# Optimization experiments

Measured on AMD Instinct MI355X. Metric: run time of the kernel, lower is better.

## Reference

```python
import jax, jax.numpy as jnp
import numpy as np

B, D1, D2, D3 = 4, 64, 64, 64
CIN, COUT = 32, 32
M1, M2, M3 = 8, 8, 8


def setup_inputs() -> dict:
    key = jax.random.key(0)
    k1, k2, k3 = jax.random.split(key, 3)
    x = jax.random.normal(k1, (B, D1, D2, D3, CIN), dtype=jnp.float32)
    # scale ~ random_normal initializer (stddev 0.05 default in keras)
    w_real = jax.random.normal(k2, (CIN, COUT, M1, M2, M3), dtype=jnp.float32) * 0.05
    w_imag = jax.random.normal(k3, (CIN, COUT, M1, M2, M3), dtype=jnp.float32) * 0.05
    return {"x": x, "w_real": w_real, "w_imag": w_imag}


def reference(x, w_real, w_imag):
    # tf.signal.fft3d transforms the innermost 3 dims of [B,D1,D2,D3,C]
    x_ft = jnp.fft.fftn(x.astype(jnp.complex64), axes=(2, 3, 4))
    # low-mode truncation over axes 1,2,3 (as in the original code)
    x_low = x_ft[:, :M1, :M2, :M3, :]                       # [B,M1,M2,M3,CIN]
    w = (w_real + 1j * w_imag).astype(jnp.complex64)         # [CIN,COUT,M1,M2,M3]
    x_low = jnp.transpose(x_low, (0, 4, 1, 2, 3))            # [B,CIN,M1,M2,M3]
    # Faithful to original: i,j of weights are summed out, k is matched.
    out_low = jnp.einsum('bcmnk,coijk->bomnk', x_low, w)     # [B,COUT,M1,M2,M3]
    out_low = jnp.transpose(out_low, (0, 2, 3, 4, 1))        # [B,M1,M2,M3,COUT]
    # zero-padded spectrum (replaces the wasteful tensor_scatter_nd_update)
    out_ft = jnp.zeros((B, D1, D2, D3, COUT), dtype=jnp.complex64)
    out_ft = out_ft.at[:, :M1, :M2, :M3, :].set(out_low)
    y = jnp.fft.ifftn(out_ft, axes=(2, 3, 4))
    return jnp.real(y).astype(jnp.float32)
```

## Files before the change

### kernel.cpp

```cpp
#include <hip/hip_runtime.h>


#define PI2F 6.28318530717958647692f

typedef float vf4 __attribute__((ext_vector_type(4)));

__device__ __forceinline__ float2 cmul(float2 a, float2 b) {
    return make_float2(a.x * b.x - a.y * b.y, a.x * b.y + a.y * b.x);
}

__global__ void k_weff(const float* __restrict__ wr, const float* __restrict__ wi,
                       float2* __restrict__ Weff) {
    __shared__ float2 ls[256];
    int t = threadIdx.x;
    int eL = t & 31, ijg = t >> 5;
    int e = blockIdx.x * 32 + eL;
    int base = (e >> 3) * 512 + (e & 7) + ijg * 64;
    float sr = 0.f, si = 0.f;
    #pragma unroll
    for (int j = 0; j < 8; ++j) { sr += wr[base + j * 8]; si += wi[base + j * 8]; }
    ls[t] = make_float2(sr, si);
    __syncthreads();
    if (t < 32) {
        float2 a = ls[t];
        #pragma unroll
        for (int g = 1; g < 8; ++g) { float2 v = ls[g * 32 + t]; a.x += v.x; a.y += v.y; }
        Weff[blockIdx.x * 32 + t] = a;
    }
}

__global__ void k_T(const float2* __restrict__ Weff, float2* __restrict__ T) {
    __shared__ float2 tw32[32];
    __shared__ float2 P[1024];
    __shared__ float2 A[256];
    int t = threadIdx.x;
    int c = blockIdx.x;
    if (t < 32) {
        float s, co_;
        __sincosf((PI2F / 32.f) * (float)t, &s, &co_);
        tw32[t] = make_float2(co_, s);
    }
    __syncthreads();
    {
        int g = t >> 8, rem = t & 255;
        float2 acc = make_float2(0.f, 0.f);
        #pragma unroll
        for (int k = 0; k < 8; ++k) {
            int fc = g * 8 + k;
            float2 v = Weff[fc * 256 + rem];
            float2 e = tw32[(fc * c) & 31];
            acc.x += v.x * e.x + v.y * e.y;
            acc.y += v.y * e.x - v.x * e.y;
        }
        P[t] = acc;
    }
    __syncthreads();
    if (t < 256) {
        float2 a = P[t];
        #pragma unroll
        for (int g = 1; g < 4; ++g) { float2 v = P[g * 256 + t]; a.x += v.x; a.y += v.y; }
        A[t] = a;
    }
    __syncthreads();
    {
        int g = t >> 8, rem = t & 255;
        int f3 = rem >> 5, co = rem & 31;
        float2 acc = make_float2(0.f, 0.f);
        #pragma unroll
        for (int k = 0; k < 8; ++k) {
            int o = g * 8 + k;
            float2 v = A[o * 8 + f3];
            float2 e = tw32[(o * co) & 31];
            acc.x += v.x * e.x - v.y * e.y;
            acc.y += v.x * e.y + v.y * e.x;
        }
        P[t] = acc;
    }
    __syncthreads();
    if (t < 256) {
        float2 a = P[t];
        #pragma unroll
        for (int g = 1; g < 4; ++g) { float2 v = P[g * 256 + t]; a.x += v.x; a.y += v.y; }
        T[c * 256 + t] = a;
    }
}

__global__ void k_dft2(const float* __restrict__ x, float2* __restrict__ S1) {
    __shared__ float2 tw64[64];
    __shared__ float2 P[2048];
    int t = threadIdx.x;
    int gid = blockIdx.x;
    int d3 = gid & 63, s = gid >> 6;
    int b = s >> 3, d1 = s & 7;
    int c = t & 31, d2g = t >> 5;
    if (t < 64) {
        float sn, cs;
        __sincosf((PI2F / 64.f) * (float)t, &sn, &cs);
        tw64[t] = make_float2(cs, sn);
    }
    __syncthreads();
    const float* xp = x + (size_t)b * 8388608 + (size_t)d1 * 131072 + d3 * 32 + c;
    float2 acc[8];
    #pragma unroll
    for (int f2 = 0; f2 < 8; ++f2) acc[f2] = make_float2(0.f, 0.f);
    #pragma unroll
    for (int k = 0; k < 8; ++k) {
        int d2 = d2g * 8 + k;
        float v = xp[d2 * 2048];
        #pragma unroll
        for (int f2 = 0; f2 < 8; ++f2) {
            float2 e = tw64[(f2 * d2) & 63];
            acc[f2].x += v * e.x;
            acc[f2].y -= v * e.y;
        }
    }
    #pragma unroll
    for (int f2 = 0; f2 < 8; ++f2) P[(d2g * 8 + f2) * 32 + c] = acc[f2];
    __syncthreads();
    {
        int f2 = t >> 5, cc = t & 31;
        float2 a = make_float2(0.f, 0.f);
        #pragma unroll
        for (int g = 0; g < 8; ++g) {
            float2 v = P[(g * 8 + f2) * 32 + cc];
            a.x += v.x; a.y += v.y;
        }
        S1[(size_t)(s * 8 + f2) * 2048 + d3 * 32 + cc] = a;
    }
}

__global__ void k_mid3(const float2* __restrict__ S1, const float2* __restrict__ T,
                       float2* __restrict__ S6) {
    __shared__ float2 sl1[2048];
    __shared__ float2 P[1024];
    __shared__ float2 s2[256];
    __shared__ float2 s5[256];
    __shared__ float2 tw[64];
    int t = threadIdx.x;
    int gid = blockIdx.x;
    if (t < 64) {
        float sn, cs;
        __sincosf((PI2F / 64.f) * (float)t, &sn, &cs);
        tw[t] = make_float2(cs, sn);
    }
    {
        const float4* src = (const float4*)(S1 + (size_t)gid * 2048);
        ((float4*)sl1)[t] = src[t];
    }
    __syncthreads();
    {
        int g = t >> 8, rem = t & 255;
        int f3 = rem >> 5, c = rem & 31;
        float2 a = make_float2(0.f, 0.f);
        #pragma unroll 4
        for (int k = 0; k < 16; ++k) {
            int d3 = g * 16 + k;
            float2 v = sl1[d3 * 32 + c];
            float2 e = tw[(f3 * d3) & 63];
            a.x += v.x * e.x + v.y * e.y;
            a.y += v.y * e.x - v.x * e.y;
        }
        P[t] = a;
    }
    __syncthreads();
    if (t < 256) {
        float2 a = P[t];
        #pragma unroll
        for (int g = 1; g < 4; ++g) { float2 v = P[g * 256 + t]; a.x += v.x; a.y += v.y; }
        s2[t] = a;
    }
    __syncthreads();
    {
        int g = t >> 8, rem = t & 255;
        int f3 = rem >> 5, co = rem & 31;
        float2 a = make_float2(0.f, 0.f);
        #pragma unroll
        for (int k = 0; k < 8; ++k) {
            int cc = g * 8 + k;
            float2 v = s2[f3 * 32 + cc];
            float2 w = T[cc * 256 + f3 * 32 + co];
            a.x += v.x * w.x - v.y * w.y;
            a.y += v.x * w.y + v.y * w.x;
        }
        P[t] = a;
    }
    __syncthreads();
    if (t < 256) {
        float2 a = P[t];
        #pragma unroll
        for (int g = 1; g < 4; ++g) { float2 v = P[g * 256 + t]; a.x += v.x; a.y += v.y; }
        s5[t] = a;
    }
    __syncthreads();
    {
        int co = t & 31, d3a = t >> 5;
        float2* outp = S6 + (size_t)gid * 2048;
        #pragma unroll
        for (int h = 0; h < 2; ++h) {
            int d3 = d3a + 32 * h;
            float2 a = make_float2(0.f, 0.f);
            #pragma unroll
            for (int f3 = 0; f3 < 8; ++f3) {
                float2 v = s5[f3 * 32 + co];
                float2 e = tw[(f3 * d3) & 63];
                a.x += v.x * e.x - v.y * e.y;
                a.y += v.x * e.y + v.y * e.x;
            }
            outp[d3 * 32 + co] = a;
        }
    }
}

__global__ void k_final2(const float2* __restrict__ S6, float* __restrict__ out) {
    __shared__ float2 ls[2048];
    __shared__ float2 tw[64];
    int t = threadIdx.x;
    int gid = blockIdx.x;
    int blk = gid & 7;
    int d1  = (gid >> 3) & 63;
    int b   = gid >> 9;
    int co4 = t & 7;
    int d3r = (t >> 3) & 7;
    int d2q = t >> 6;
    float* obase = out + (size_t)b * 8388608 + (size_t)d1 * 131072
                 + (blk * 8 + d3r) * 32 + co4 * 4;
    if (d1 >= 8) {
        vf4 z = {0.f, 0.f, 0.f, 0.f};
        #pragma unroll
        for (int i = 0; i < 16; ++i) {
            int d2 = d2q * 16 + i;
            __builtin_nontemporal_store(z, (vf4*)(obase + d2 * 2048));
        }
        return;
    }
    if (t < 64) {
        float sn, cs;
        __sincosf((PI2F / 64.f) * (float)t, &sn, &cs);
        tw[t] = make_float2(cs, sn);
    }
    {
        const float4* src = (const float4*)(S6 + (size_t)(b * 8 + d1) * 16384);
        float4* dst = (float4*)ls;
        #pragma unroll
        for (int j = 0; j < 4; ++j) {
            int i4 = t + j * 256;
            int f2 = i4 >> 7, rem = i4 & 127;
            dst[i4] = src[f2 * 1024 + blk * 128 + rem];
        }
    }
    __syncthreads();
    float2 v[8][4];
    #pragma unroll
    for (int f2 = 0; f2 < 8; ++f2) {
        #pragma unroll
        for (int k = 0; k < 4; ++k)
            v[f2][k] = ls[f2 * 256 + d3r * 32 + co4 * 4 + k];
    }
    const float sc = 1.f / 131072.f;
    #pragma unroll 2
    for (int i = 0; i < 16; ++i) {
        int d2 = d2q * 16 + i;
        float rx = 0.f, ry = 0.f, rz = 0.f, rw = 0.f;
        #pragma unroll
        for (int f2 = 0; f2 < 8; ++f2) {
            float2 e = tw[(f2 * d2) & 63];
            rx += v[f2][0].x * e.x - v[f2][0].y * e.y;
            ry += v[f2][1].x * e.x - v[f2][1].y * e.y;
            rz += v[f2][2].x * e.x - v[f2][2].y * e.y;
            rw += v[f2][3].x * e.x - v[f2][3].y * e.y;
        }
        vf4 r = {rx * sc, ry * sc, rz * sc, rw * sc};
        __builtin_nontemporal_store(r, (vf4*)(obase + d2 * 2048));
    }
}

extern "C" void kernel_launch(void* const* d_in, const int* in_sizes, int n_in,
                              void* d_out, int out_size, void* d_ws, size_t ws_size,
                              hipStream_t stream) {
    const float* x  = (const float*)d_in[0];
    const float* wr = (const float*)d_in[1];
    const float* wi = (const float*)d_in[2];
    float* out = (float*)d_out;

    float2* Weff = (float2*)d_ws;
    float2* T    = Weff + 8192;
    float2* S1   = T + 8192;
    float2* S6   = S1 + 524288;

    k_weff  <<<256,  256,  0, stream>>>(wr, wi, Weff);
    k_T     <<<32,   1024, 0, stream>>>(Weff, T);
    k_dft2  <<<2048, 256,  0, stream>>>(x, S1);
    k_mid3  <<<256,  1024, 0, stream>>>(S1, T, S6);
    k_final2<<<2048, 256,  0, stream>>>(S6, out);
}
```

Baseline: 222.9 us.

## Move inverse d3 DFT from mix kernel into final kernel, shrinking intermediate

The inverse DFT along the third spatial axis is moved out of the mode-mixing kernel and into the final output kernel. The mixing kernel now writes only the 8 low modes per slice, a 256-entry buffer instead of 2048, which cuts intermediate global traffic roughly eightfold. The final kernel loads the compact modes and expands the 8 d3 positions for its block in shared memory before the d2 expansion. This adds a second shared buffer and some redundant per-block recomputation in the final kernel.

```diff
diff --git a/kernel.cpp b/kernel.cpp
--- a/kernel.cpp
+++ b/kernel.cpp
@@ -4,10 +4,6 @@
 #define PI2F 6.28318530717958647692f
 
 typedef float vf4 __attribute__((ext_vector_type(4)));
-
-__device__ __forceinline__ float2 cmul(float2 a, float2 b) {
-    return make_float2(a.x * b.x - a.y * b.y, a.x * b.y + a.y * b.x);
-}
 
 __global__ void k_weff(const float* __restrict__ wr, const float* __restrict__ wi,
                        float2* __restrict__ Weff) {
@@ -129,12 +125,11 @@
     }
 }
 
-__global__ void k_mid3(const float2* __restrict__ S1, const float2* __restrict__ T,
-                       float2* __restrict__ S6) {
+__global__ void k_mix(const float2* __restrict__ S1, const float2* __restrict__ T,
+                      float2* __restrict__ s5g) {
     __shared__ float2 sl1[2048];
     __shared__ float2 P[1024];
     __shared__ float2 s2[256];
-    __shared__ float2 s5[256];
     __shared__ float2 tw[64];
     int t = threadIdx.x;
     int gid = blockIdx.x;
@@ -189,30 +184,13 @@
         float2 a = P[t];
         #pragma unroll
         for (int g = 1; g < 4; ++g) { float2 v = P[g * 256 + t]; a.x += v.x; a.y += v.y; }
-        s5[t] = a;
-    }
-    __syncthreads();
-    {
-        int co = t & 31, d3a = t >> 5;
-        float2* outp = S6 + (size_t)gid * 2048;
-        #pragma unroll
-        for (int h = 0; h < 2; ++h) {
-            int d3 = d3a + 32 * h;
-            float2 a = make_float2(0.f, 0.f);
-            #pragma unroll
-            for (int f3 = 0; f3 < 8; ++f3) {
-                float2 v = s5[f3 * 32 + co];
-                float2 e = tw[(f3 * d3) & 63];
-                a.x += v.x * e.x - v.y * e.y;
-                a.y += v.x * e.y + v.y * e.x;
-            }
-            outp[d3 * 32 + co] = a;
-        }
-    }
-}
-
-__global__ void k_final2(const float2* __restrict__ S6, float* __restrict__ out) {
-    __shared__ float2 ls[2048];
+        s5g[(size_t)gid * 256 + t] = a;
+    }
+}
+
+__global__ void k_final3(const float2* __restrict__ s5g, float* __restrict__ out) {
+    __shared__ float2 ls5[2048];
+    __shared__ float2 sq6[2048];
     __shared__ float2 tw[64];
     int t = threadIdx.x;
     int gid = blockIdx.x;
@@ -220,10 +198,10 @@
     int d1  = (gid >> 3) & 63;
     int b   = gid >> 9;
     int co4 = t & 7;
-    int d3r = (t >> 3) & 7;
+    int d3r8 = (t >> 3) & 7;
     int d2q = t >> 6;
     float* obase = out + (size_t)b * 8388608 + (size_t)d1 * 131072
-                 + (blk * 8 + d3r) * 32 + co4 * 4;
+                 + (blk * 8 + d3r8) * 32 + co4 * 4;
     if (d1 >= 8) {
         vf4 z = {0.f, 0.f, 0.f, 0.f};
         #pragma unroll
@@ -239,13 +217,26 @@
         tw[t] = make_float2(cs, sn);
     }
     {
-        const float4* src = (const float4*)(S6 + (size_t)(b * 8 + d1) * 16384);
-        float4* dst = (float4*)ls;
-        #pragma unroll
-        for (int j = 0; j < 4; ++j) {
-            int i4 = t + j * 256;
-            int f2 = i4 >> 7, rem = i4 & 127;
-            dst[i4] = src[f2 * 1024 + blk * 128 + rem];
+        const float4* src = (const float4*)(s5g + (size_t)(b * 8 + d1) * 2048);
+        float4* dst = (float4*)ls5;
+        #pragma unroll
+        for (int j = 0; j < 4; ++j) dst[t + j * 256] = src[t + j * 256];
+    }
+    __syncthreads();
+    {
+        int co = t & 31, d3r = t >> 5;
+        int d3 = blk * 8 + d3r;
+        #pragma unroll
+        for (int f2 = 0; f2 < 8; ++f2) {
+            float2 a = make_float2(0.f, 0.f);
+            #pragma unroll
+            for (int f3 = 0; f3 < 8; ++f3) {
+                float2 v = ls5[f2 * 256 + f3 * 32 + co];
+                float2 e = tw[(f3 * d3) & 63];
+                a.x += v.x * e.x - v.y * e.y;
+                a.y += v.x * e.y + v.y * e.x;
+            }
+            sq6[f2 * 256 + d3r * 32 + co] = a;
         }
     }
     __syncthreads();
@@ -254,7 +245,7 @@
     for (int f2 = 0; f2 < 8; ++f2) {
         #pragma unroll
         for (int k = 0; k < 4; ++k)
-            v[f2][k] = ls[f2 * 256 + d3r * 32 + co4 * 4 + k];
+            v[f2][k] = sq6[f2 * 256 + d3r8 * 32 + co4 * 4 + k];
     }
     const float sc = 1.f / 131072.f;
     #pragma unroll 2
@@ -285,11 +276,11 @@
     float2* Weff = (float2*)d_ws;
     float2* T    = Weff + 8192;
     float2* S1   = T + 8192;
-    float2* S6   = S1 + 524288;
+    float2* s5g  = S1 + 524288;
 
     k_weff  <<<256,  256,  0, stream>>>(wr, wi, Weff);
     k_T     <<<32,   1024, 0, stream>>>(Weff, T);
     k_dft2  <<<2048, 256,  0, stream>>>(x, S1);
-    k_mid3  <<<256,  1024, 0, stream>>>(S1, T, S6);
-    k_final2<<<2048, 256,  0, stream>>>(S6, out);
-}
+    k_mix   <<<256,  1024, 0, stream>>>(S1, T, s5g);
+    k_final3<<<2048, 256,  0, stream>>>(s5g, out);
+}
```

New measurement: 222.6 us. Within noise of the previous version (-0.1%).
